# Kernel optimization log

Hardware: AMD Instinct MI355X
Metric: run time of the kernel (lower is better)

The kernel has to match this reference:

```python
import jax, jax.numpy as jnp
import numpy as np

# RoIAlign config (matches init_kwargs)
OUT_H, OUT_W = 7, 7
SPATIAL_SCALE = 0.25
SAMPLE_NUM = 2  # sampling points per bin side (static)


def setup_inputs() -> dict:
    key = jax.random.key(0)
    k0, k1, k2, k3 = jax.random.split(key, 4)
    B, C, H, W = 2, 256, 200, 336
    N = 1024
    img_h, img_w = H / SPATIAL_SCALE, W / SPATIAL_SCALE
    features = jax.random.normal(k0, (B, C, H, W), dtype=jnp.float32)
    # build valid rois: [batch_idx, x1, y1, x2, y2] in image coordinates
    bidx = jax.random.randint(k1, (N,), 0, B).astype(jnp.float32)
    ctr = jax.random.uniform(k2, (N, 2)) * jnp.array([img_w, img_h], jnp.float32)
    wh = (0.05 + 0.35 * jax.random.uniform(k3, (N, 2))) * jnp.array([img_w, img_h], jnp.float32)
    x1y1 = jnp.clip(ctr - wh / 2, 0.0)
    x2y2 = jnp.minimum(ctr + wh / 2, jnp.array([img_w, img_h], jnp.float32))
    rois = jnp.concatenate([bidx[:, None], x1y1[:, 0:1], x1y1[:, 1:2], x2y2[:, 0:1], x2y2[:, 1:2]], axis=1)
    return {"features": features, "rois": rois}


def _roi_align(features, rois):
    B, C, H, W = features.shape
    N = rois.shape[0]
    ns = SAMPLE_NUM
    P, Q = OUT_H * ns, OUT_W * ns  # full sampling grid per roi

    bidx = rois[:, 0].astype(jnp.int32)
    x1 = rois[:, 1] * SPATIAL_SCALE
    y1 = rois[:, 2] * SPATIAL_SCALE
    x2 = rois[:, 3] * SPATIAL_SCALE
    y2 = rois[:, 4] * SPATIAL_SCALE
    roi_w = jnp.maximum(x2 - x1, 1.0)  # aligned=False legacy semantics
    roi_h = jnp.maximum(y2 - y1, 1.0)
    bin_w = roi_w / OUT_W
    bin_h = roi_h / OUT_H

    # sample coords: y = y1 + (p + 0.5) * bin_h / ns, p in [0, P)
    ys = y1[:, None] + (jnp.arange(P, dtype=jnp.float32) + 0.5) * (bin_h[:, None] / ns)  # (N,P)
    xs = x1[:, None] + (jnp.arange(Q, dtype=jnp.float32) + 0.5) * (bin_w[:, None] / ns)  # (N,Q)

    # out-of-bound samples contribute zero (kernel skips y<-1 or y>H)
    ymask = (ys >= -1.0) & (ys <= H)
    xmask = (xs >= -1.0) & (xs <= W)
    y = jnp.clip(ys, 0.0, H - 1)
    x = jnp.clip(xs, 0.0, W - 1)
    y0 = jnp.floor(y).astype(jnp.int32)
    x0 = jnp.floor(x).astype(jnp.int32)
    y1i = jnp.minimum(y0 + 1, H - 1)
    x1i = jnp.minimum(x0 + 1, W - 1)
    ly = y - y0.astype(jnp.float32)
    lx = x - x0.astype(jnp.float32)
    hy, hx = 1.0 - ly, 1.0 - lx

    b = bidx[:, None, None]            # (N,1,1)
    def gather(yi, xi):                # -> (N,P,Q,C)
        return features[b, :, yi[:, :, None], xi[:, None, :]]
    f00 = gather(y0, x0)
    f01 = gather(y0, x1i)
    f10 = gather(y1i, x0)
    f11 = gather(y1i, x1i)

    wy0, wy1 = hy[:, :, None, None], ly[:, :, None, None]  # (N,P,1,1)
    wx0, wx1 = hx[:, None, :, None], lx[:, None, :, None]  # (N,1,Q,1)
    val = wy0 * (wx0 * f00 + wx1 * f01) + wy1 * (wx0 * f10 + wx1 * f11)
    val = val * (ymask[:, :, None, None] & xmask[:, None, :, None])

    # average the ns x ns samples per output bin
    val = val.reshape(N, OUT_H, ns, OUT_W, ns, C).mean(axis=(2, 4))  # (N,OUT_H,OUT_W,C)
    return jnp.transpose(val, (0, 3, 1, 2))  # (N,C,OUT_H,OUT_W)


def reference(features, rois):
    return _roi_align(features, rois)
```

## Files before the change

kernel.cpp:

```cpp
#include <hip/hip_runtime.h>
#include <hip/hip_fp16.h>

#define BB   2
#define CCH  256
#define HH   200
#define WW   336
#define HWN  (HH * WW)
#define OH   7
#define OW   7
#define SCALEF 0.25f
#define NBIN (OH * OW)
#define PER_ROI (CCH * NBIN)
#define NBANDS 8
#define NBUCK (BB * NBANDS)

typedef float  nfloat4 __attribute__((ext_vector_type(4)));

__device__ __forceinline__ __half2 u32_as_h2(unsigned int u) {
    union { unsigned int u; __half2 h; } c;
    c.u = u;
    return c.h;
}

__global__ __launch_bounds__(256) void transpose_f16_k(const float* __restrict__ src,
                                                       unsigned short* __restrict__ dst,
                                                       const float* __restrict__ rois,
                                                       int N, int* __restrict__ perm) {
    __shared__ float tile[64][65];
    __shared__ int cnt[NBUCK], off[NBUCK];
    __shared__ unsigned char keys[1024];

    const int tx  = threadIdx.x;
    const int ty  = threadIdx.y;
    const int tid = ty * 16 + tx;

    if (blockIdx.x == 0 && blockIdx.y == 0 && blockIdx.z == 0) {
        if (N > 1024 || N < 8) {
            for (int i = tid; i < N; i += 256) perm[i] = i;
        } else {
            if (tid < NBUCK) cnt[tid] = 0;
            __syncthreads();
            for (int i = tid; i < N; i += 256) {
                const float* r = rois + i * 5;
                const int b = (int)r[0];
                const float yc = (r[2] + r[4]) * 0.5f * SCALEF;
                int band = (int)(yc * ((float)NBANDS / (float)HH));
                band = min(max(band, 0), NBANDS - 1);
                const int k = b * NBANDS + band;
                keys[i] = (unsigned char)k;
                atomicAdd(&cnt[k], 1);
            }
            __syncthreads();
            if (tid == 0) {
                int s = 0;
                for (int k = 0; k < NBUCK; ++k) { off[k] = s; s += cnt[k]; }
            }
            __syncthreads();
            for (int i = tid; i < N; i += 256) {
                perm[atomicAdd(&off[keys[i]], 1)] = i;
            }
        }
        __syncthreads();
    }

    const int b   = blockIdx.z;
    const int hw0 = blockIdx.x * 64;
    const int c0  = blockIdx.y * 64;

#pragma unroll
    for (int r = 0; r < 4; ++r) {
        const int cl = ty + r * 16;
        const nfloat4 v = __builtin_nontemporal_load(
            (const nfloat4*)(src + (size_t)(b * CCH + c0 + cl) * HWN + hw0 + tx * 4));
        tile[cl][tx * 4 + 0] = v.x;
        tile[cl][tx * 4 + 1] = v.y;
        tile[cl][tx * 4 + 2] = v.z;
        tile[cl][tx * 4 + 3] = v.w;
    }
    __syncthreads();
#pragma unroll
    for (int r = 0; r < 4; ++r) {
        const int hwl = ty + r * 16;
        ushort4 o;
        o.x = __half_as_ushort(__float2half(tile[tx * 4 + 0][hwl]));
        o.y = __half_as_ushort(__float2half(tile[tx * 4 + 1][hwl]));
        o.z = __half_as_ushort(__float2half(tile[tx * 4 + 2][hwl]));
        o.w = __half_as_ushort(__float2half(tile[tx * 4 + 3][hwl]));
        *(ushort4*)(dst + (size_t)(b * HWN + hw0 + hwl) * CCH + c0 + tx * 4) = o;
    }
}

__global__ __launch_bounds__(512, 8) void roi_align_f16_k(const unsigned short* __restrict__ f,
                                                          const float* __restrict__ rois,
                                                          const int* __restrict__ perm,
                                                          float* __restrict__ out) {
    const int nblk = gridDim.x;
    int p;
    if ((nblk & 7) == 0) {
        p = (blockIdx.x & 7) * (nblk >> 3) + (blockIdx.x >> 3);
    } else {
        p = blockIdx.x;
    }
    const int n    = perm[p];
    const int tid  = threadIdx.x;
    const int lane = tid & 63;
    const int half = lane >> 5;
    const int l32  = lane & 31;
    const int g    = tid >> 6;
    const int c8   = l32 * 8;

    __shared__ __align__(16) unsigned short buf_h[PER_ROI];
    __shared__ int   s_yb0[14], s_yb1[14];
    __shared__ int   s_xb0[14], s_xb1[14];
    __shared__ float s_ly[14],  s_lx[14];
    __shared__ float s_vy[14],  s_vx[14];

    const float* r = rois + n * 5;
    const int   b   = (int)r[0];
    const float rx1 = r[1] * SCALEF, ry1 = r[2] * SCALEF;
    const float rx2 = r[3] * SCALEF, ry2 = r[4] * SCALEF;
    const float bw = fmaxf(rx2 - rx1, 1.0f) * (1.0f / OW);
    const float bh = fmaxf(ry2 - ry1, 1.0f) * (1.0f / OH);

    if (tid < 14) {
        const float ys = ry1 + ((float)tid + 0.5f) * (bh * 0.5f);
        s_vy[tid] = (ys >= -1.0f && ys <= (float)HH) ? 1.0f : 0.0f;
        const float y = fminf(fmaxf(ys, 0.0f), (float)(HH - 1));
        const int y0  = (int)floorf(y);
        const int y1  = min(y0 + 1, HH - 1);
        s_yb0[tid] = (b * HH + y0) * (WW * CCH);
        s_yb1[tid] = (b * HH + y1) * (WW * CCH);
        s_ly[tid]  = y - (float)y0;
    } else if (tid >= 64 && tid < 78) {
        const int j = tid - 64;
        const float xs = rx1 + ((float)j + 0.5f) * (bw * 0.5f);
        s_vx[j] = (xs >= -1.0f && xs <= (float)WW) ? 1.0f : 0.0f;
        const float x = fminf(fmaxf(xs, 0.0f), (float)(WW - 1));
        const int x0  = (int)floorf(x);
        const int x1  = min(x0 + 1, WW - 1);
        s_xb0[j] = x0 * CCH;
        s_xb1[j] = x1 * CCH;
        s_lx[j]  = x - (float)x0;
    }
    __syncthreads();

    const unsigned short* fp = f + c8;

    for (int bin = g; bin < NBIN; bin += 8) {
        const int ph = bin / OW;
        const int pw = bin - ph * OW;
        float acc[8] = {0.f, 0.f, 0.f, 0.f, 0.f, 0.f, 0.f, 0.f};
#pragma unroll
        for (int ix = 0; ix < 2; ++ix) {
            const int px  = pw * 2 + ix;
            const int xbs = half ? s_xb1[px] : s_xb0[px];
            const float wxs = (half ? s_lx[px] : (1.0f - s_lx[px]))
                              * s_vx[px] * 0.25f;
#pragma unroll
            for (int iy = 0; iy < 2; ++iy) {
                const int py = ph * 2 + iy;
                const float ly = s_ly[py];
                const float m  = wxs * s_vy[py];
                const uint4 q0 = *(const uint4*)(fp + s_yb0[py] + xbs);
                const uint4 q1 = *(const uint4*)(fp + s_yb1[py] + xbs);
                const __half2 W0 = __float2half2_rn(m * (1.0f - ly));
                const __half2 W1 = __float2half2_rn(m * ly);
                const __half2 v0 = __hfma2(W1, u32_as_h2(q1.x), __hmul2(W0, u32_as_h2(q0.x)));
                const __half2 v1 = __hfma2(W1, u32_as_h2(q1.y), __hmul2(W0, u32_as_h2(q0.y)));
                const __half2 v2 = __hfma2(W1, u32_as_h2(q1.z), __hmul2(W0, u32_as_h2(q0.z)));
                const __half2 v3 = __hfma2(W1, u32_as_h2(q1.w), __hmul2(W0, u32_as_h2(q0.w)));
                acc[0] += __low2float(v0);  acc[1] += __high2float(v0);
                acc[2] += __low2float(v1);  acc[3] += __high2float(v1);
                acc[4] += __low2float(v2);  acc[5] += __high2float(v2);
                acc[6] += __low2float(v3);  acc[7] += __high2float(v3);
            }
        }
#pragma unroll
        for (int j = 0; j < 8; ++j) {
            acc[j] += __shfl_xor(acc[j], 32);
        }
#pragma unroll
        for (int j = 0; j < 8; ++j) {
            buf_h[(c8 + j) * NBIN + bin] = __half_as_ushort(__float2half(acc[j]));
        }
    }
    __syncthreads();

    nfloat4* ob = (nfloat4*)(out + (size_t)n * PER_ROI);
    const uint2* bb = (const uint2*)buf_h;
    for (int i = tid; i < PER_ROI / 4; i += 512) {
        const uint2 q = bb[i];
        const __half2 a = u32_as_h2(q.x), c = u32_as_h2(q.y);
        nfloat4 v;
        v.x = __low2float(a);  v.y = __high2float(a);
        v.z = __low2float(c);  v.w = __high2float(c);
        __builtin_nontemporal_store(v, ob + i);
    }
}

__global__ __launch_bounds__(256) void roi_align_direct_k(const float* __restrict__ f,
                                                          const float* __restrict__ rois,
                                                          float* __restrict__ out) {
    const int n   = blockIdx.x;
    const int c   = threadIdx.x;

    __shared__ int   s_y0[14], s_y1[14], s_x0[14], s_x1[14];
    __shared__ float s_ly[14], s_lx[14], s_vy[14], s_vx[14];

    const float* r = rois + n * 5;
    const int   b   = (int)r[0];
    const float rx1 = r[1] * SCALEF, ry1 = r[2] * SCALEF;
    const float rx2 = r[3] * SCALEF, ry2 = r[4] * SCALEF;
    const float bw = fmaxf(rx2 - rx1, 1.0f) * (1.0f / OW);
    const float bh = fmaxf(ry2 - ry1, 1.0f) * (1.0f / OH);

    if (c < 14) {
        const float ys = ry1 + ((float)c + 0.5f) * (bh * 0.5f);
        s_vy[c] = (ys >= -1.0f && ys <= (float)HH) ? 1.0f : 0.0f;
        const float y = fminf(fmaxf(ys, 0.0f), (float)(HH - 1));
        const int y0  = (int)floorf(y);
        s_y0[c] = y0 * WW;
        s_y1[c] = min(y0 + 1, HH - 1) * WW;
        s_ly[c] = y - (float)y0;
    } else if (c >= 64 && c < 78) {
        const int j = c - 64;
        const float xs = rx1 + ((float)j + 0.5f) * (bw * 0.5f);
        s_vx[j] = (xs >= -1.0f && xs <= (float)WW) ? 1.0f : 0.0f;
        const float x = fminf(fmaxf(xs, 0.0f), (float)(WW - 1));
        const int x0  = (int)floorf(x);
        s_x0[j] = x0;
        s_x1[j] = min(x0 + 1, WW - 1);
        s_lx[j] = x - (float)x0;
    }
    __syncthreads();

    const float* fb = f + (size_t)(b * CCH + c) * HWN;
    for (int bin = 0; bin < NBIN; ++bin) {
        const int ph = bin / OW, pw = bin - ph * OW;
        float acc = 0.0f;
        for (int iy = 0; iy < 2; ++iy) {
            const int py = ph * 2 + iy;
            const float ly = s_ly[py], hy = 1.0f - ly;
            for (int ix = 0; ix < 2; ++ix) {
                const int px = pw * 2 + ix;
                const float lx = s_lx[px], hx = 1.0f - lx;
                const float m = s_vy[py] * s_vx[px] * 0.25f;
                acc += m * (hy * (hx * fb[s_y0[py] + s_x0[px]] + lx * fb[s_y0[py] + s_x1[px]]) +
                            ly * (hx * fb[s_y1[py] + s_x0[px]] + lx * fb[s_y1[py] + s_x1[px]]));
            }
        }
        out[(size_t)n * PER_ROI + c * NBIN + bin] = acc;
    }
}

extern "C" void kernel_launch(void* const* d_in, const int* in_sizes, int n_in,
                              void* d_out, int out_size, void* d_ws, size_t ws_size,
                              hipStream_t stream) {
    const float* feat = (const float*)d_in[0];
    const float* rois = (const float*)d_in[1];
    float* out = (float*)d_out;
    const int N = in_sizes[1] / 5;

    const size_t tensor_bytes = (size_t)BB * CCH * HWN * sizeof(unsigned short);
    const size_t need = tensor_bytes + (size_t)N * sizeof(int);
    if (ws_size >= need) {
        unsigned short* fcl = (unsigned short*)d_ws;
        int* perm = (int*)((char*)d_ws + tensor_bytes);
        transpose_f16_k<<<dim3(HWN / 64, CCH / 64, BB), dim3(16, 16), 0, stream>>>(
            feat, fcl, rois, N, perm);
        roi_align_f16_k<<<N, 512, 0, stream>>>(fcl, rois, perm, out);
    } else {
        roi_align_direct_k<<<N, 256, 0, stream>>>(feat, rois, out);
    }
}
```

Measured before the change: 239.5 us.

## Split RoI channels across two blocks and give each lane one bilinear corner

The RoI kernel grid gains a second dimension that splits the 256 channels into two halves of 128. Each block now needs half the shared-memory staging buffer, which should allow more resident blocks. Within a wave, each 16-lane group handles one of the four bilinear corners and loads only that corner, and the corners are combined with two cross-lane shuffles. Interpolation also moves from half-precision FMAs to fp32 multiply-adds. The cost is twice as many blocks, each repeating the RoI coordinate setup, plus an extra shuffle stage.

Result: no change. 237.7 us (-0.8%).

```diff
diff --git a/kernel.cpp b/kernel.cpp
--- a/kernel.cpp
+++ b/kernel.cpp
@@ -13,6 +13,8 @@
 #define PER_ROI (CCH * NBIN)
 #define NBANDS 8
 #define NBUCK (BB * NBANDS)
+#define CHALF 128
+#define HALF_OUT (CHALF * NBIN)
 
 typedef float  nfloat4 __attribute__((ext_vector_type(4)));
 
@@ -102,14 +104,16 @@
         p = blockIdx.x;
     }
     const int n    = perm[p];
+    const int cb   = blockIdx.y;
     const int tid  = threadIdx.x;
     const int lane = tid & 63;
-    const int half = lane >> 5;
-    const int l32  = lane & 31;
+    const int l16  = lane & 15;
+    const int qx   = (lane >> 4) & 1;
+    const int qy   = lane >> 5;
     const int g    = tid >> 6;
-    const int c8   = l32 * 8;
-
-    __shared__ __align__(16) unsigned short buf_h[PER_ROI];
+    const int c8   = l16 * 8;
+
+    __shared__ __align__(16) unsigned short buf_h[HALF_OUT];
     __shared__ int   s_yb0[14], s_yb1[14];
     __shared__ int   s_xb0[14], s_xb1[14];
     __shared__ float s_ly[14],  s_lx[14];
@@ -144,7 +148,7 @@
     }
     __syncthreads();
 
-    const unsigned short* fp = f + c8;
+    const unsigned short* fp = f + cb * CHALF + c8;
 
     for (int bin = g; bin < NBIN; bin += 8) {
         const int ph = bin / OW;
@@ -152,31 +156,30 @@
         float acc[8] = {0.f, 0.f, 0.f, 0.f, 0.f, 0.f, 0.f, 0.f};
 #pragma unroll
         for (int ix = 0; ix < 2; ++ix) {
-            const int px  = pw * 2 + ix;
-            const int xbs = half ? s_xb1[px] : s_xb0[px];
-            const float wxs = (half ? s_lx[px] : (1.0f - s_lx[px]))
-                              * s_vx[px] * 0.25f;
+            const int px   = pw * 2 + ix;
+            const int xbs  = qx ? s_xb1[px] : s_xb0[px];
+            const float lx = s_lx[px];
+            const float wx = (qx ? lx : (1.0f - lx)) * s_vx[px] * 0.25f;
 #pragma unroll
             for (int iy = 0; iy < 2; ++iy) {
-                const int py = ph * 2 + iy;
+                const int py   = ph * 2 + iy;
+                const int ybs  = qy ? s_yb1[py] : s_yb0[py];
                 const float ly = s_ly[py];
-                const float m  = wxs * s_vy[py];
-                const uint4 q0 = *(const uint4*)(fp + s_yb0[py] + xbs);
-                const uint4 q1 = *(const uint4*)(fp + s_yb1[py] + xbs);
-                const __half2 W0 = __float2half2_rn(m * (1.0f - ly));
-                const __half2 W1 = __float2half2_rn(m * ly);
-                const __half2 v0 = __hfma2(W1, u32_as_h2(q1.x), __hmul2(W0, u32_as_h2(q0.x)));
-                const __half2 v1 = __hfma2(W1, u32_as_h2(q1.y), __hmul2(W0, u32_as_h2(q0.y)));
-                const __half2 v2 = __hfma2(W1, u32_as_h2(q1.z), __hmul2(W0, u32_as_h2(q0.z)));
-                const __half2 v3 = __hfma2(W1, u32_as_h2(q1.w), __hmul2(W0, u32_as_h2(q0.w)));
-                acc[0] += __low2float(v0);  acc[1] += __high2float(v0);
-                acc[2] += __low2float(v1);  acc[3] += __high2float(v1);
-                acc[4] += __low2float(v2);  acc[5] += __high2float(v2);
-                acc[6] += __low2float(v3);  acc[7] += __high2float(v3);
+                const float w  = wx * (qy ? ly : (1.0f - ly)) * s_vy[py];
+                const uint4 q = *(const uint4*)(fp + ybs + xbs);
+                const float2 f0 = __half22float2(u32_as_h2(q.x));
+                const float2 f1 = __half22float2(u32_as_h2(q.y));
+                const float2 f2 = __half22float2(u32_as_h2(q.z));
+                const float2 f3 = __half22float2(u32_as_h2(q.w));
+                acc[0] += w * f0.x;  acc[1] += w * f0.y;
+                acc[2] += w * f1.x;  acc[3] += w * f1.y;
+                acc[4] += w * f2.x;  acc[5] += w * f2.y;
+                acc[6] += w * f3.x;  acc[7] += w * f3.y;
             }
         }
 #pragma unroll
         for (int j = 0; j < 8; ++j) {
+            acc[j] += __shfl_xor(acc[j], 16);
             acc[j] += __shfl_xor(acc[j], 32);
         }
 #pragma unroll
@@ -186,9 +189,9 @@
     }
     __syncthreads();
 
-    nfloat4* ob = (nfloat4*)(out + (size_t)n * PER_ROI);
+    nfloat4* ob = (nfloat4*)(out + (size_t)n * PER_ROI + cb * HALF_OUT);
     const uint2* bb = (const uint2*)buf_h;
-    for (int i = tid; i < PER_ROI / 4; i += 512) {
+    for (int i = tid; i < HALF_OUT / 4; i += 512) {
         const uint2 q = bb[i];
         const __half2 a = u32_as_h2(q.x), c = u32_as_h2(q.y);
         nfloat4 v;
@@ -268,7 +271,7 @@
         int* perm = (int*)((char*)d_ws + tensor_bytes);
         transpose_f16_k<<<dim3(HWN / 64, CCH / 64, BB), dim3(16, 16), 0, stream>>>(
             feat, fcl, rois, N, perm);
-        roi_align_f16_k<<<N, 512, 0, stream>>>(fcl, rois, perm, out);
+        roi_align_f16_k<<<dim3(N, 2), 512, 0, stream>>>(fcl, rois, perm, out);
     } else {
         roi_align_direct_k<<<N, 256, 0, stream>>>(feat, rois, out);
     }
```
